# Kernel optimization log

Hardware: AMD Instinct MI355X
Metric: run time of the kernel (lower is better)

## Reference

```python
import jax, jax.numpy as jnp
import numpy as np
from jax import lax

_A = -0.75  # PyTorch bicubic coefficient


def _cubic_kernel(x):
    x = np.abs(x)
    return np.where(x <= 1.0, (_A + 2) * x**3 - (_A + 3) * x**2 + 1,
                    np.where(x < 2.0, _A * x**3 - 5 * _A * x**2 + 8 * _A * x - 4 * _A, 0.0))


def _cubic_mat(out_s, in_s):
    # align_corners=True bicubic interpolation matrix [out_s, in_s]
    i = np.arange(out_s)
    s = i * (in_s - 1) / (out_s - 1) if out_s > 1 else np.zeros(out_s)
    f = np.floor(s).astype(np.int64)
    t = s - f
    M = np.zeros((out_s, in_s), dtype=np.float32)
    for off in range(-1, 3):
        idx = np.clip(f + off, 0, in_s - 1)
        np.add.at(M, (i, idx), _cubic_kernel(t - off).astype(np.float32))
    return jnp.asarray(M)


def _bicubic_up(x, out_hw):
    Mh = _cubic_mat(out_hw[0], x.shape[-2])
    Mw = _cubic_mat(out_hw[1], x.shape[-1])
    y = jnp.einsum('Hh,bchw->bcHw', Mh, x)
    return jnp.einsum('Ww,bcHw->bcHW', Mw, y)


def _conv(x, w, b, pad=1):
    y = lax.conv_general_dilated(x, w, (1, 1), [(pad, pad), (pad, pad)],
                                 dimension_numbers=('NCHW', 'OIHW', 'NCHW'))
    return y + b[None, :, None, None]


def _pool(x):
    return lax.reduce_window(x, -jnp.inf, lax.max, (1, 1, 2, 2), (1, 1, 2, 2), 'VALID')


def _features(x, ws):
    # VGG19 feat1 = conv0+relu (64ch, full res); feat2 = conv2..conv14 (256ch, 1/4 res)
    x1 = jax.nn.relu(_conv(x, *ws[0]))
    h = jax.nn.relu(_conv(x1, *ws[1]))
    h = _pool(h)
    h = jax.nn.relu(_conv(h, *ws[2]))
    h = jax.nn.relu(_conv(h, *ws[3]))
    h = _pool(h)
    h = jax.nn.relu(_conv(h, *ws[4]))
    h = jax.nn.relu(_conv(h, *ws[5]))
    h = jax.nn.relu(_conv(h, *ws[6]))
    h = _bicubic_up(h, x1.shape[-2:])  # bicubic, align_corners=True
    return jnp.concatenate([x1, h], axis=1)  # 64 + 256 = 320 channels


def _forward(x_ref, x_template, w0, b0, w2, b2, w5, b5, w7, b7, w10, b10, w12, b12,
             w14, b14, coef_ref, coef_temp, fw1, fb1, fw2, fb2, fw3, fb3):
    ws = [(w0, b0), (w2, b2), (w5, b5), (w7, b7), (w10, b10), (w12, b12), (w14, b14)]
    fref = _features(x_ref, ws)
    ftem = _features(x_template, ws)
    # L2-normalize over channel dim
    fref = fref / (1e-8 + jnp.linalg.norm(fref, axis=1, keepdims=True))
    ftem = ftem / (1e-8 + jnp.linalg.norm(ftem, axis=1, keepdims=True))
    b, c, H, W = fref.shape
    fref = fref.reshape(b, c, H // 2, 2, W // 2, 2).mean(axis=(3, 5))
    # dense correlation volume
    dist = jnp.einsum('bcmn,bcpq->bmnpq', fref, ftem) / 320.0
    m, n, p, q = dist.shape[1:]
    dist = dist.reshape(b, m * n, p * q)
    # dual-axis softmax + sqrt combination (LoFTR-style)
    conf_ref = jax.nn.softmax(coef_ref * dist, axis=-2)
    conf_tmp = jax.nn.softmax(coef_temp * dist, axis=-1)
    confidence = jnp.sqrt(conf_ref * conf_tmp)
    conf_values, _ = lax.top_k(confidence, 5)  # [b, m*n, 5]
    conf = conf_values.reshape(b, m, n, 5).transpose(0, 3, 1, 2)
    # final head (dropout = identity in eval)
    h = jax.nn.relu(_conv(conf, fw1, fb1))
    h = jax.nn.relu(_conv(h, fw2, fb2))
    out = _conv(h, fw3, fb3, pad=0)
    out = _bicubic_up(out, x_ref.shape[-2:])
    return out


def setup_inputs() -> dict:
    key = jax.random.key(0)
    ks = jax.random.split(key, 16)
    B, H, W = 1, 128, 128

    def cw(k, o, i, s):
        return jax.random.normal(k, (o, i, s, s), jnp.float32) * (1.0 / np.sqrt(i * s * s))

    d = {
        'x_ref': jax.random.normal(ks[0], (B, 3, H, W), jnp.float32),
        'x_template': jax.random.normal(ks[1], (B, 3, H, W), jnp.float32),
        'w0': cw(ks[2], 64, 3, 3), 'b0': jnp.zeros((64,), jnp.float32),
        'w2': cw(ks[3], 64, 64, 3), 'b2': jnp.zeros((64,), jnp.float32),
        'w5': cw(ks[4], 128, 64, 3), 'b5': jnp.zeros((128,), jnp.float32),
        'w7': cw(ks[5], 128, 128, 3), 'b7': jnp.zeros((128,), jnp.float32),
        'w10': cw(ks[6], 256, 128, 3), 'b10': jnp.zeros((256,), jnp.float32),
        'w12': cw(ks[7], 256, 256, 3), 'b12': jnp.zeros((256,), jnp.float32),
        'w14': cw(ks[8], 256, 256, 3), 'b14': jnp.zeros((256,), jnp.float32),
        'coef_ref': jnp.float32(1.0), 'coef_temp': jnp.float32(1.0),
        # final head: weights_init_normal -> N(1/3, 0.02)
        'fw1': 1.0 / 3 + 0.02 * jax.random.normal(ks[9], (8, 5, 3, 3), jnp.float32),
        'fb1': 0.02 * jax.random.normal(ks[10], (8,), jnp.float32),
        'fw2': 1.0 / 3 + 0.02 * jax.random.normal(ks[11], (8, 8, 3, 3), jnp.float32),
        'fb2': 0.02 * jax.random.normal(ks[12], (8,), jnp.float32),
        'fw3': 1.0 / 3 + 0.02 * jax.random.normal(ks[13], (1, 8, 1, 1), jnp.float32),
        'fb3': 0.02 * jax.random.normal(ks[14], (1,), jnp.float32),
    }
    return d


def reference(x_ref, x_template, w0, b0, w2, b2, w5, b5, w7, b7, w10, b10, w12, b12,
              w14, b14, coef_ref, coef_temp, fw1, fb1, fw2, fb2, fw3, fb3):
    return _forward(x_ref, x_template, w0, b0, w2, b2, w5, b5, w7, b7, w10, b10,
                    w12, b12, w14, b14, coef_ref, coef_temp, fw1, fb1, fw2, fb2, fw3, fb3)
```

## Files before the change

kernel.cpp:

```cpp
#include <hip/hip_runtime.h>
#include <math.h>

typedef unsigned short ushort_t;
typedef unsigned int uint_t;
typedef __attribute__((ext_vector_type(8))) short bf16x8;
typedef __attribute__((ext_vector_type(4))) float f32x4;

#define FSTRIDE ((size_t)16384 * 320)
#define TSTRIDE ((size_t)16384 * 64)

__device__ inline ushort_t f2bf(float f) {
    union { float f; uint_t u; } x; x.f = f;
    uint_t r = x.u + 0x7fffu + ((x.u >> 16) & 1u);
    return (ushort_t)(r >> 16);
}
__device__ inline float bf2f(ushort_t h) {
    union { uint_t u; float f; } x; x.u = ((uint_t)h) << 16;
    return x.f;
}
__device__ inline float bflo(uint_t u) {
    union { uint_t u; float f; } x; x.u = u << 16; return x.f;
}
__device__ inline float bfhi(uint_t u) {
    union { uint_t u; float f; } x; x.u = u & 0xffff0000u; return x.f;
}

__global__ void wtrans_k(const float* __restrict__ w, ushort_t* __restrict__ wT, int CO, int CI)
{
    int idx = blockIdx.x * 256 + threadIdx.x;
    if (idx >= CO * CI * 9) return;
    int tap = idx % 9;
    int rem = idx / 9;
    int ci = rem % CI;
    int co = rem / CI;
    wT[((size_t)tap * CO + co) * CI + ci] = f2bf(w[idx]);
}

__global__ __launch_bounds__(256) void conv0_k(const float* __restrict__ x0, const float* __restrict__ x1,
                                               const float* __restrict__ w,
                                               const float* __restrict__ b, ushort_t* __restrict__ F)
{
    const float* x = blockIdx.y ? x1 : x0;
    F += (size_t)blockIdx.y * FSTRIDE;
    int co = threadIdx.x & 63;
    int p = blockIdx.x * 4 + (threadIdx.x >> 6);
    int y = p >> 7, xx = p & 127;
    float acc = b[co];
#pragma unroll
    for (int ci = 0; ci < 3; ++ci) {
#pragma unroll
        for (int t = 0; t < 9; ++t) {
            int dy = t / 3 - 1, dx = t % 3 - 1;
            int yy = y + dy, xc = xx + dx;
            if ((unsigned)yy < 128u && (unsigned)xc < 128u) {
                acc += x[ci * 16384 + yy * 128 + xc] * w[co * 27 + ci * 9 + t];
            }
        }
    }
    F[(size_t)p * 320 + co] = f2bf(fmaxf(acc, 0.f));
}

template<int CI>
__global__ __launch_bounds__(256) void conv_mfma_k(
    const ushort_t* __restrict__ in, int ldin, int inoff, size_t inImgStride,
    const ushort_t* __restrict__ wT, const float* __restrict__ bias,
    ushort_t* __restrict__ out, int ldout, int outoff, size_t outImgStride,
    int H, int W, int CO)
{
    in += (size_t)blockIdx.z * inImgStride;
    out += (size_t)blockIdx.z * outImgStride;
    const int tid = threadIdx.x;
    const int lane = tid & 63, wid = tid >> 6;
    const int wr = wid >> 1, wc = wid & 1;
    const int m0 = blockIdx.x * 64;
    const int n0 = blockIdx.y * 64;
    const int fr = lane & 15;
    const int fo = (lane >> 4) << 3;

    size_t abase[2];
    unsigned vmask[2];
#pragma unroll
    for (int mi = 0; mi < 2; ++mi) {
        int p = m0 + wr * 32 + mi * 16 + fr;
        int y = p / W, x = p % W;
        abase[mi] = (size_t)p * ldin + inoff + fo;
        unsigned vm = 0;
#pragma unroll
        for (int t = 0; t < 9; ++t) {
            int dy = t / 3 - 1, dx = t % 3 - 1;
            if ((unsigned)(y + dy) < (unsigned)H && (unsigned)(x + dx) < (unsigned)W) vm |= 1u << t;
        }
        vmask[mi] = vm;
    }

    f32x4 zero = {0.f, 0.f, 0.f, 0.f};
    f32x4 acc[2][2] = {{zero, zero}, {zero, zero}};
    const bf16x8 zz = {0, 0, 0, 0, 0, 0, 0, 0};

    for (int t = 0; t < 9; ++t) {
        int toff = ((t / 3 - 1) * W + (t % 3 - 1)) * ldin;
        bool v0 = (vmask[0] >> t) & 1u;
        bool v1 = (vmask[1] >> t) & 1u;
        const ushort_t* wp0 = wT + ((size_t)(t * CO + n0 + wc * 32 + fr)) * CI + fo;
        const ushort_t* wp1 = wp0 + (size_t)16 * CI;
#pragma unroll
        for (int kc = 0; kc < CI / 32; ++kc) {
            int k0 = kc * 32;
            bf16x8 a0 = v0 ? *(const bf16x8*)(in + abase[0] + toff + k0) : zz;
            bf16x8 a1 = v1 ? *(const bf16x8*)(in + abase[1] + toff + k0) : zz;
            bf16x8 b0 = *(const bf16x8*)(wp0 + k0);
            bf16x8 b1 = *(const bf16x8*)(wp1 + k0);
            acc[0][0] = __builtin_amdgcn_mfma_f32_16x16x32_bf16(a0, b0, acc[0][0], 0, 0, 0);
            acc[0][1] = __builtin_amdgcn_mfma_f32_16x16x32_bf16(a0, b1, acc[0][1], 0, 0, 0);
            acc[1][0] = __builtin_amdgcn_mfma_f32_16x16x32_bf16(a1, b0, acc[1][0], 0, 0, 0);
            acc[1][1] = __builtin_amdgcn_mfma_f32_16x16x32_bf16(a1, b1, acc[1][1], 0, 0, 0);
        }
    }

#pragma unroll
    for (int mi = 0; mi < 2; ++mi) {
#pragma unroll
        for (int ni = 0; ni < 2; ++ni) {
            int row0 = m0 + wr * 32 + mi * 16 + ((lane >> 4) << 2);
            int col = n0 + wc * 32 + ni * 16 + (lane & 15);
            float bv = bias[col];
#pragma unroll
            for (int r = 0; r < 4; ++r)
                out[(size_t)(row0 + r) * ldout + outoff + col] = f2bf(fmaxf(acc[mi][ni][r] + bv, 0.f));
        }
    }
}

__global__ void maxpool_nhwc_k(const ushort_t* __restrict__ in, ushort_t* __restrict__ out,
                               int C, int Hi, int Wi)
{
    in += (size_t)blockIdx.y * TSTRIDE;
    out += (size_t)blockIdx.y * TSTRIDE;
    int idx = blockIdx.x * 256 + threadIdx.x;
    int CG = C >> 3;
    int Wo = Wi >> 1, Ho = Hi >> 1;
    if (idx >= Ho * Wo * CG) return;
    int cg = idx % CG;
    int p = idx / CG;
    int y = p / Wo, x = p % Wo;
    const ushort_t* ip = in + ((size_t)(2 * y) * Wi + 2 * x) * C + cg * 8;
    bf16x8 v0 = *(const bf16x8*)(ip);
    bf16x8 v1 = *(const bf16x8*)(ip + C);
    bf16x8 v2 = *(const bf16x8*)(ip + (size_t)Wi * C);
    bf16x8 v3 = *(const bf16x8*)(ip + (size_t)Wi * C + C);
    bf16x8 r;
#pragma unroll
    for (int j = 0; j < 8; ++j) {
        float m = fmaxf(fmaxf(bf2f((ushort_t)v0[j]), bf2f((ushort_t)v1[j])),
                        fmaxf(bf2f((ushort_t)v2[j]), bf2f((ushort_t)v3[j])));
        r[j] = (short)f2bf(m);
    }
    *(bf16x8*)(out + (size_t)p * C + cg * 8) = r;
}

__device__ inline void cubw(float t, float* w) {
    float x0 = 1.f + t, x2 = 1.f - t, x3 = 2.f - t;
    w[0] = ((-0.75f*x0 + 3.75f)*x0 - 6.f)*x0 + 3.f;
    w[1] = (1.25f*t - 2.25f)*t*t + 1.f;
    w[2] = (1.25f*x2 - 2.25f)*x2*x2 + 1.f;
    w[3] = ((-0.75f*x3 + 3.75f)*x3 - 6.f)*x3 + 3.f;
}

__global__ __launch_bounds__(256) void bicubic_nhwc_k(const ushort_t* __restrict__ in, ushort_t* __restrict__ F)
{
    in += (size_t)blockIdx.y * TSTRIDE;
    F += (size_t)blockIdx.y * FSTRIDE;
    int idx = blockIdx.x * 256 + threadIdx.x;
    int cg = idx & 31;
    int p = idx >> 5;
    int Y = p >> 7, X = p & 127;
    float sy = (float)Y * (31.f / 127.f);
    float sx = (float)X * (31.f / 127.f);
    int fy = (int)floorf(sy), fx = (int)floorf(sx);
    float ty = sy - (float)fy, tx = sx - (float)fx;
    float wy[4], wx[4];
    cubw(ty, wy); cubw(tx, wx);
    float a[8] = {0.f, 0.f, 0.f, 0.f, 0.f, 0.f, 0.f, 0.f};
#pragma unroll
    for (int i = 0; i < 4; ++i) {
        int yy = min(max(fy - 1 + i, 0), 31);
#pragma unroll
        for (int j = 0; j < 4; ++j) {
            int xx = min(max(fx - 1 + j, 0), 31);
            float w = wy[i] * wx[j];
            bf16x8 v = *(const bf16x8*)(in + ((size_t)yy * 32 + xx) * 256 + cg * 8);
#pragma unroll
            for (int e = 0; e < 8; ++e) a[e] += w * bf2f((ushort_t)v[e]);
        }
    }
    bf16x8 r;
#pragma unroll
    for (int e = 0; e < 8; ++e) r[e] = (short)f2bf(a[e]);
    *(bf16x8*)(F + (size_t)p * 320 + 64 + cg * 8) = r;
}

__global__ __launch_bounds__(256) void norm_k(ushort_t* __restrict__ F)
{
    int lane = threadIdx.x & 63;
    int p = blockIdx.x * 4 + (threadIdx.x >> 6);
    ushort_t* rp = F + (size_t)p * 320;
    bool act = lane < 40;
    bf16x8 v = {0, 0, 0, 0, 0, 0, 0, 0};
    float ss = 0.f;
    if (act) {
        v = *(const bf16x8*)(rp + lane * 8);
#pragma unroll
        for (int e = 0; e < 8; ++e) { float f = bf2f((ushort_t)v[e]); ss += f * f; }
    }
#pragma unroll
    for (int off = 32; off > 0; off >>= 1) ss += __shfl_xor(ss, off);
    float inv = 1.f / (1e-8f + sqrtf(ss));
    if (act) {
#pragma unroll
        for (int e = 0; e < 8; ++e) v[e] = (short)f2bf(bf2f((ushort_t)v[e]) * inv);
        *(bf16x8*)(rp + lane * 8) = v;
    }
}

__global__ void pool_ref_nhwc_k(const ushort_t* __restrict__ F, ushort_t* __restrict__ A)
{
    int idx = blockIdx.x * 256 + threadIdx.x;
    if (idx >= 4096 * 40) return;
    int cg = idx % 40;
    int m = idx / 40;
    int y = m >> 6, x = m & 63;
    const ushort_t* ip = F + ((size_t)(2 * y) * 128 + 2 * x) * 320 + cg * 8;
    bf16x8 v0 = *(const bf16x8*)(ip);
    bf16x8 v1 = *(const bf16x8*)(ip + 320);
    bf16x8 v2 = *(const bf16x8*)(ip + 128 * 320);
    bf16x8 v3 = *(const bf16x8*)(ip + 128 * 320 + 320);
    bf16x8 r;
#pragma unroll
    for (int j = 0; j < 8; ++j) {
        float s = bf2f((ushort_t)v0[j]) + bf2f((ushort_t)v1[j]) + bf2f((ushort_t)v2[j]) + bf2f((ushort_t)v3[j]);
        r[j] = (short)f2bf(0.25f * s);
    }
    *(bf16x8*)(A + (size_t)m * 320 + cg * 8) = r;
}

__global__ __launch_bounds__(256) void gemm_corr_k(
    const ushort_t* __restrict__ A, const ushort_t* __restrict__ B, ushort_t* __restrict__ D,
    const float* __restrict__ coefr, const float* __restrict__ coeft,
    float* __restrict__ rpsum, float* __restrict__ cpsum)
{
    __shared__ ushort_t lA[128 * 32];
    __shared__ ushort_t lB[128 * 32];
    __shared__ float cl[2][128];
    __shared__ float rl[2][128];
    const int tid = threadIdx.x;
    const int lane = tid & 63;
    const int wid = tid >> 6;
    const int wr = wid >> 1, wc = wid & 1;
    const int m0 = blockIdx.y * 128, n0 = blockIdx.x * 128;
    const int rS = tid >> 2;
    const int cS = (tid & 3) << 3;
    const int fr = lane & 15;
    const int fo = (lane >> 4) << 3;

    f32x4 zero = {0.f, 0.f, 0.f, 0.f};
    f32x4 acc[4][4];
#pragma unroll
    for (int i = 0; i < 4; ++i)
#pragma unroll
        for (int j = 0; j < 4; ++j) acc[i][j] = zero;

    for (int k0 = 0; k0 < 320; k0 += 32) {
        uint4 a0 = *(const uint4*)(A + (size_t)(m0 + rS) * 320 + k0 + cS);
        uint4 a1 = *(const uint4*)(A + (size_t)(m0 + 64 + rS) * 320 + k0 + cS);
        uint4 b0 = *(const uint4*)(B + (size_t)(n0 + rS) * 320 + k0 + cS);
        uint4 b1 = *(const uint4*)(B + (size_t)(n0 + 64 + rS) * 320 + k0 + cS);
        __syncthreads();
        *(uint4*)&lA[rS * 32 + cS] = a0;
        *(uint4*)&lA[(64 + rS) * 32 + cS] = a1;
        *(uint4*)&lB[rS * 32 + cS] = b0;
        *(uint4*)&lB[(64 + rS) * 32 + cS] = b1;
        __syncthreads();
        bf16x8 af[4], bfr[4];
#pragma unroll
        for (int mi = 0; mi < 4; ++mi)
            af[mi] = *(const bf16x8*)&lA[(wr * 64 + mi * 16 + fr) * 32 + fo];
#pragma unroll
        for (int ni = 0; ni < 4; ++ni)
            bfr[ni] = *(const bf16x8*)&lB[(wc * 64 + ni * 16 + fr) * 32 + fo];
#pragma unroll
        for (int mi = 0; mi < 4; ++mi)
#pragma unroll
            for (int ni = 0; ni < 4; ++ni)
                acc[mi][ni] = __builtin_amdgcn_mfma_f32_16x16x32_bf16(af[mi], bfr[ni], acc[mi][ni], 0, 0, 0);
    }

    const float s = 1.0f / 320.0f;
    const float cr = coefr[0], ct = coeft[0];
    float cp[4] = {0.f, 0.f, 0.f, 0.f};
    float rp[4][4];
#pragma unroll
    for (int mi = 0; mi < 4; ++mi)
#pragma unroll
        for (int r = 0; r < 4; ++r) rp[mi][r] = 0.f;

#pragma unroll
    for (int mi = 0; mi < 4; ++mi) {
#pragma unroll
        for (int ni = 0; ni < 4; ++ni) {
            int grow0 = m0 + wr * 64 + mi * 16 + ((lane >> 4) << 2);
            int gcol = n0 + wc * 64 + ni * 16 + (lane & 15);
#pragma unroll
            for (int r = 0; r < 4; ++r) {
                float d = acc[mi][ni][r] * s;
                D[(size_t)(grow0 + r) * 16384 + gcol] = f2bf(d);
                cp[ni] += __expf(cr * d);
                rp[mi][r] += __expf(ct * d);
            }
        }
    }
#pragma unroll
    for (int ni = 0; ni < 4; ++ni) {
        cp[ni] += __shfl_xor(cp[ni], 16);
        cp[ni] += __shfl_xor(cp[ni], 32);
    }
    if (lane < 16) {
#pragma unroll
        for (int ni = 0; ni < 4; ++ni)
            cl[wr][wc * 64 + ni * 16 + lane] = cp[ni];
    }
#pragma unroll
    for (int mi = 0; mi < 4; ++mi)
#pragma unroll
        for (int r = 0; r < 4; ++r) {
            rp[mi][r] += __shfl_xor(rp[mi][r], 1);
            rp[mi][r] += __shfl_xor(rp[mi][r], 2);
            rp[mi][r] += __shfl_xor(rp[mi][r], 4);
            rp[mi][r] += __shfl_xor(rp[mi][r], 8);
        }
    if ((lane & 15) == 0) {
        int g = lane >> 4;
#pragma unroll
        for (int mi = 0; mi < 4; ++mi)
#pragma unroll
            for (int r = 0; r < 4; ++r)
                rl[wc][wr * 64 + mi * 16 + g * 4 + r] = rp[mi][r];
    }
    __syncthreads();
    if (tid < 128) {
        cpsum[(size_t)blockIdx.y * 16384 + n0 + tid] = cl[0][tid] + cl[1][tid];
        rpsum[(size_t)blockIdx.x * 4096 + m0 + tid] = rl[0][tid] + rl[1][tid];
    }
}

__global__ void colfin_k(const float* __restrict__ cpsum, float* __restrict__ lc)
{
    int j = blockIdx.x * 256 + threadIdx.x;
    float s = 0.f;
#pragma unroll
    for (int k = 0; k < 32; ++k) s += cpsum[(size_t)k * 16384 + j];
    lc[j] = -0.5f * __logf(s);
}
__global__ void rowfin_k(const float* __restrict__ rpsum, float* __restrict__ invr)
{
    int m = blockIdx.x * 256 + threadIdx.x;
    float s = 0.f;
#pragma unroll
    for (int k = 0; k < 128; ++k) s += rpsum[(size_t)k * 4096 + m];
    invr[m] = rsqrtf(s);
}

#define INS5(w_) { float w = (w_); float mx; \
    mx = fmaxf(w, t0); w = fminf(w, t0); t0 = mx; \
    mx = fmaxf(w, t1); w = fminf(w, t1); t1 = mx; \
    mx = fmaxf(w, t2); w = fminf(w, t2); t2 = mx; \
    mx = fmaxf(w, t3); w = fminf(w, t3); t3 = mx; \
    t4 = fmaxf(w, t4); }

__global__ __launch_bounds__(256) void row_topk_k(
    const ushort_t* __restrict__ Dist, const float* __restrict__ lc,
    const float* __restrict__ invr,
    const float* __restrict__ coefr, const float* __restrict__ coeft,
    float* __restrict__ conf5)
{
    int wid = threadIdx.x >> 6, lane = threadIdx.x & 63;
    int row = blockIdx.x * 4 + wid;
    float hc = 0.5f * (coefr[0] + coeft[0]);
    const ushort_t* rp = Dist + (size_t)row * 16384;

    float t0 = -1e30f, t1 = -1e30f, t2 = -1e30f, t3 = -1e30f, t4 = -1e30f;
    for (int i = 0; i < 32; ++i) {
        int col = (i * 64 + lane) * 8;
        uint4 u = *(const uint4*)(rp + col);
        float4 l0 = *(const float4*)(lc + col);
        float4 l1 = *(const float4*)(lc + col + 4);
        INS5(fmaf(hc, bflo(u.x), l0.x));
        INS5(fmaf(hc, bfhi(u.x), l0.y));
        INS5(fmaf(hc, bflo(u.y), l0.z));
        INS5(fmaf(hc, bfhi(u.y), l0.w));
        INS5(fmaf(hc, bflo(u.z), l1.x));
        INS5(fmaf(hc, bfhi(u.z), l1.y));
        INS5(fmaf(hc, bflo(u.w), l1.z));
        INS5(fmaf(hc, bfhi(u.w), l1.w));
    }
#pragma unroll
    for (int off = 1; off < 64; off <<= 1) {
        float o0 = __shfl_xor(t0, off), o1 = __shfl_xor(t1, off), o2 = __shfl_xor(t2, off);
        float o3 = __shfl_xor(t3, off), o4 = __shfl_xor(t4, off);
        INS5(o0); INS5(o1); INS5(o2); INS5(o3); INS5(o4);
    }
    if (lane == 0) {
        float iv = invr[row];
        conf5[0 * 4096 + row] = __expf(t0) * iv;
        conf5[1 * 4096 + row] = __expf(t1) * iv;
        conf5[2 * 4096 + row] = __expf(t2) * iv;
        conf5[3 * 4096 + row] = __expf(t3) * iv;
        conf5[4 * 4096 + row] = __expf(t4) * iv;
    }
}

__global__ void conv3x3_k(const float* __restrict__ in, const float* __restrict__ wgt,
                          const float* __restrict__ bias, float* __restrict__ out,
                          int Cin, int H, int W, int relu)
{
    int p = blockIdx.x * 256 + threadIdx.x;
    int HW = H * W;
    if (p >= HW) return;
    int co0 = blockIdx.y * 8;
    int y = p / W, x = p - y * W;
    float acc0 = bias[co0+0], acc1 = bias[co0+1], acc2 = bias[co0+2], acc3 = bias[co0+3];
    float acc4 = bias[co0+4], acc5 = bias[co0+5], acc6 = bias[co0+6], acc7 = bias[co0+7];
    bool ym = y > 0, yp = y < H-1, xm = x > 0, xp = x < W-1;
    for (int ci = 0; ci < Cin; ++ci) {
        const float* ip = in + (size_t)ci * HW + p;
        float v0 = (ym && xm) ? ip[-W-1] : 0.f;
        float v1 = (ym)       ? ip[-W]   : 0.f;
        float v2 = (ym && xp) ? ip[-W+1] : 0.f;
        float v3 = (xm)       ? ip[-1]   : 0.f;
        float v4 =              ip[0];
        float v5 = (xp)       ? ip[1]    : 0.f;
        float v6 = (yp && xm) ? ip[W-1]  : 0.f;
        float v7 = (yp)       ? ip[W]    : 0.f;
        float v8 = (yp && xp) ? ip[W+1]  : 0.f;
        const float* wp = wgt + ((size_t)co0 * Cin + ci) * 9;
        size_t ws = (size_t)Cin * 9;
#define CACC(q, a) { const float* wq = wp + q * ws; \
        a += wq[0]*v0 + wq[1]*v1 + wq[2]*v2 + wq[3]*v3 + wq[4]*v4 \
           + wq[5]*v5 + wq[6]*v6 + wq[7]*v7 + wq[8]*v8; }
        CACC(0, acc0) CACC(1, acc1) CACC(2, acc2) CACC(3, acc3)
        CACC(4, acc4) CACC(5, acc5) CACC(6, acc6) CACC(7, acc7)
#undef CACC
    }
#define CW(q, a) { float r = a; if (relu) r = fmaxf(r, 0.f); out[(size_t)(co0+q)*HW + p] = r; }
    CW(0, acc0) CW(1, acc1) CW(2, acc2) CW(3, acc3)
    CW(4, acc4) CW(5, acc5) CW(6, acc6) CW(7, acc7)
#undef CW
}

__global__ void bicubic_k(const float* __restrict__ in, float* __restrict__ out,
                          int C, int Hin, int Win, int Hout, int Wout)
{
    int idx = blockIdx.x * 256 + threadIdx.x;
    int total = C * Hout * Wout;
    if (idx >= total) return;
    int X = idx % Wout;
    int Y = (idx / Wout) % Hout;
    int c = idx / (Wout * Hout);
    float sy = (float)Y * (float)(Hin - 1) / (float)(Hout - 1);
    float sx = (float)X * (float)(Win - 1) / (float)(Wout - 1);
    int fy = (int)floorf(sy), fx = (int)floorf(sx);
    float ty = sy - (float)fy, tx = sx - (float)fx;
    float wy[4], wx[4];
    cubw(ty, wy); cubw(tx, wx);
    const float* ip = in + (size_t)c * Hin * Win;
    float acc = 0.f;
#pragma unroll
    for (int i = 0; i < 4; ++i) {
        int yy = min(max(fy - 1 + i, 0), Hin - 1);
        float ra = 0.f;
#pragma unroll
        for (int j = 0; j < 4; ++j) {
            int xx = min(max(fx - 1 + j, 0), Win - 1);
            ra += wx[j] * ip[yy * Win + xx];
        }
        acc += wy[i] * ra;
    }
    out[idx] = acc;
}

__global__ void conv1x1_k(const float* __restrict__ in, const float* __restrict__ w,
                          const float* __restrict__ b, float* __restrict__ out, int Cin, int HW)
{
    int p = blockIdx.x * 256 + threadIdx.x;
    if (p >= HW) return;
    float a = b[0];
    for (int c = 0; c < Cin; ++c) a += w[c] * in[(size_t)c * HW + p];
    out[p] = a;
}

extern "C" void kernel_launch(void* const* d_in, const int* in_sizes, int n_in,
                              void* d_out, int out_size, void* d_ws, size_t ws_size,
                              hipStream_t stream)
{
    const float* x_ref = (const float*)d_in[0];
    const float* x_tem = (const float*)d_in[1];
    const float* w0  = (const float*)d_in[2];   const float* b0  = (const float*)d_in[3];
    const float* w2  = (const float*)d_in[4];   const float* b2  = (const float*)d_in[5];
    const float* w5  = (const float*)d_in[6];   const float* b5  = (const float*)d_in[7];
    const float* w7  = (const float*)d_in[8];   const float* b7  = (const float*)d_in[9];
    const float* w10 = (const float*)d_in[10];  const float* b10 = (const float*)d_in[11];
    const float* w12 = (const float*)d_in[12];  const float* b12 = (const float*)d_in[13];
    const float* w14 = (const float*)d_in[14];  const float* b14 = (const float*)d_in[15];
    const float* coefr = (const float*)d_in[16];
    const float* coeft = (const float*)d_in[17];
    const float* fw1 = (const float*)d_in[18];  const float* fb1 = (const float*)d_in[19];
    const float* fw2 = (const float*)d_in[20];  const float* fb2 = (const float*)d_in[21];
    const float* fw3 = (const float*)d_in[22];  const float* fb3 = (const float*)d_in[23];
    float* out = (float*)d_out;

    char* wsp = (char*)d_ws;
    auto alloc = [&](size_t bytes) { char* p = wsp; wsp += (bytes + 255) & ~(size_t)255; return p; };
    ushort_t* F     = (ushort_t*)alloc(2 * FSTRIDE * 2);
    ushort_t* t1    = (ushort_t*)alloc(2 * TSTRIDE * 2);
    ushort_t* t2    = (ushort_t*)alloc(2 * TSTRIDE * 2);
    ushort_t* wT2   = (ushort_t*)alloc((size_t)64 * 64 * 9 * 2);
    ushort_t* wT5   = (ushort_t*)alloc((size_t)128 * 64 * 9 * 2);
    ushort_t* wT7   = (ushort_t*)alloc((size_t)128 * 128 * 9 * 2);
    ushort_t* wT10  = (ushort_t*)alloc((size_t)256 * 128 * 9 * 2);
    ushort_t* wT12  = (ushort_t*)alloc((size_t)256 * 256 * 9 * 2);
    ushort_t* wT14  = (ushort_t*)alloc((size_t)256 * 256 * 9 * 2);
    ushort_t* Abuf  = (ushort_t*)alloc((size_t)4096 * 320 * 2);
    ushort_t* dist  = (ushort_t*)alloc((size_t)4096 * 16384 * 2);
    float*    rpsum = (float*)alloc((size_t)128 * 4096 * 4);
    float*    cpsum = (float*)alloc((size_t)32 * 16384 * 4);
    float*    lc    = (float*)alloc(16384 * 4);
    float*    invr  = (float*)alloc(4096 * 4);
    float*    conf5 = (float*)alloc(5 * 4096 * 4);
    float*    h1    = (float*)alloc(8 * 4096 * 4);
    float*    h2    = (float*)alloc(8 * 4096 * 4);
    float*    out64 = (float*)alloc(4096 * 4);
    (void)ws_size; (void)n_in; (void)in_sizes; (void)out_size;

    wtrans_k<<<(64*64*9 + 255)/256, 256, 0, stream>>>(w2, wT2, 64, 64);
    wtrans_k<<<(128*64*9 + 255)/256, 256, 0, stream>>>(w5, wT5, 128, 64);
    wtrans_k<<<(128*128*9 + 255)/256, 256, 0, stream>>>(w7, wT7, 128, 128);
    wtrans_k<<<(256*128*9 + 255)/256, 256, 0, stream>>>(w10, wT10, 256, 128);
    wtrans_k<<<(256*256*9 + 255)/256, 256, 0, stream>>>(w12, wT12, 256, 256);
    wtrans_k<<<(256*256*9 + 255)/256, 256, 0, stream>>>(w14, wT14, 256, 256);

    conv0_k<<<dim3(4096, 2), 256, 0, stream>>>(x_ref, x_tem, w0, b0, F);
    conv_mfma_k<64><<<dim3(256, 1, 2), 256, 0, stream>>>(F, 320, 0, FSTRIDE, wT2, b2, t1, 64, 0, TSTRIDE, 128, 128, 64);
    maxpool_nhwc_k<<<dim3(128, 2), 256, 0, stream>>>(t1, t2, 64, 128, 128);
    conv_mfma_k<64><<<dim3(64, 2, 2), 256, 0, stream>>>(t2, 64, 0, TSTRIDE, wT5, b5, t1, 128, 0, TSTRIDE, 64, 64, 128);
    conv_mfma_k<128><<<dim3(64, 2, 2), 256, 0, stream>>>(t1, 128, 0, TSTRIDE, wT7, b7, t2, 128, 0, TSTRIDE, 64, 64, 128);
    maxpool_nhwc_k<<<dim3(64, 2), 256, 0, stream>>>(t2, t1, 128, 64, 64);
    conv_mfma_k<128><<<dim3(16, 4, 2), 256, 0, stream>>>(t1, 128, 0, TSTRIDE, wT10, b10, t2, 256, 0, TSTRIDE, 32, 32, 256);
    conv_mfma_k<256><<<dim3(16, 4, 2), 256, 0, stream>>>(t2, 256, 0, TSTRIDE, wT12, b12, t1, 256, 0, TSTRIDE, 32, 32, 256);
    conv_mfma_k<256><<<dim3(16, 4, 2), 256, 0, stream>>>(t1, 256, 0, TSTRIDE, wT14, b14, t2, 256, 0, TSTRIDE, 32, 32, 256);
    bicubic_nhwc_k<<<dim3(2048, 2), 256, 0, stream>>>(t2, F);
    norm_k<<<8192, 256, 0, stream>>>(F);

    pool_ref_nhwc_k<<<640, 256, 0, stream>>>(F, Abuf);

    gemm_corr_k<<<dim3(128, 32), 256, 0, stream>>>(Abuf, F + FSTRIDE, dist, coefr, coeft, rpsum, cpsum);

    colfin_k<<<64, 256, 0, stream>>>(cpsum, lc);
    rowfin_k<<<16, 256, 0, stream>>>(rpsum, invr);

    row_topk_k<<<1024, 256, 0, stream>>>(dist, lc, invr, coefr, coeft, conf5);

    conv3x3_k<<<dim3(16, 1), 256, 0, stream>>>(conf5, fw1, fb1, h1, 5, 64, 64, 1);
    conv3x3_k<<<dim3(16, 1), 256, 0, stream>>>(h1, fw2, fb2, h2, 8, 64, 64, 1);
    conv1x1_k<<<16, 256, 0, stream>>>(h2, fw3, fb3, out64, 8, 4096);
    bicubic_k<<<64, 256, 0, stream>>>(out64, out, 1, 64, 64, 128, 128);
}
```

Baseline: 417.1 us.

## Transpose MFMA operands for vectorized stores, use direct-to-LDS loads in correlation GEMM

Swaps the A/B operands of the MFMA calls so each lane holds four consecutive output channels, which allows packed 8-byte stores of the bf16 conv outputs and of the correlation matrix instead of scattered 2-byte stores. The correlation GEMM now stages tiles with global_load_lds, bypassing registers, and adds a trailing barrier per k-step. When both coefficients are equal it reuses one set of exponentials for the row and column sums. The 1/4-resolution convs move to a new single-wave-per-block kernel with many more, smaller blocks to raise parallelism on the small 32x32 layers.

```diff
diff --git a/kernel.cpp b/kernel.cpp
--- a/kernel.cpp
+++ b/kernel.cpp
@@ -23,6 +23,16 @@
 }
 __device__ inline float bfhi(uint_t u) {
     union { uint_t u; float f; } x; x.u = u & 0xffff0000u; return x.f;
+}
+__device__ inline uint_t cvtpk_bf16(float lo, float hi) {
+    uint_t r;
+    asm volatile("v_cvt_pk_bf16_f32 %0, %1, %2" : "=v"(r) : "v"(lo), "v"(hi));
+    return r;
+}
+__device__ inline void gload16(const void* g, void* l) {
+    __builtin_amdgcn_global_load_lds(
+        (const __attribute__((address_space(1))) void*)g,
+        (__attribute__((address_space(3))) void*)l, 16, 0, 0);
 }
 
 __global__ void wtrans_k(const float* __restrict__ w, ushort_t* __restrict__ wT, int CO, int CI)
@@ -110,10 +120,10 @@
             bf16x8 a1 = v1 ? *(const bf16x8*)(in + abase[1] + toff + k0) : zz;
             bf16x8 b0 = *(const bf16x8*)(wp0 + k0);
             bf16x8 b1 = *(const bf16x8*)(wp1 + k0);
-            acc[0][0] = __builtin_amdgcn_mfma_f32_16x16x32_bf16(a0, b0, acc[0][0], 0, 0, 0);
-            acc[0][1] = __builtin_amdgcn_mfma_f32_16x16x32_bf16(a0, b1, acc[0][1], 0, 0, 0);
-            acc[1][0] = __builtin_amdgcn_mfma_f32_16x16x32_bf16(a1, b0, acc[1][0], 0, 0, 0);
-            acc[1][1] = __builtin_amdgcn_mfma_f32_16x16x32_bf16(a1, b1, acc[1][1], 0, 0, 0);
+            acc[0][0] = __builtin_amdgcn_mfma_f32_16x16x32_bf16(b0, a0, acc[0][0], 0, 0, 0);
+            acc[0][1] = __builtin_amdgcn_mfma_f32_16x16x32_bf16(b1, a0, acc[0][1], 0, 0, 0);
+            acc[1][0] = __builtin_amdgcn_mfma_f32_16x16x32_bf16(b0, a1, acc[1][0], 0, 0, 0);
+            acc[1][1] = __builtin_amdgcn_mfma_f32_16x16x32_bf16(b1, a1, acc[1][1], 0, 0, 0);
         }
     }
 
@@ -121,12 +131,91 @@
     for (int mi = 0; mi < 2; ++mi) {
 #pragma unroll
         for (int ni = 0; ni < 2; ++ni) {
-            int row0 = m0 + wr * 32 + mi * 16 + ((lane >> 4) << 2);
-            int col = n0 + wc * 32 + ni * 16 + (lane & 15);
-            float bv = bias[col];
-#pragma unroll
-            for (int r = 0; r < 4; ++r)
-                out[(size_t)(row0 + r) * ldout + outoff + col] = f2bf(fmaxf(acc[mi][ni][r] + bv, 0.f));
+            int pix = m0 + wr * 32 + mi * 16 + (lane & 15);
+            int ch = n0 + wc * 32 + ni * 16 + ((lane >> 4) << 2);
+            float4 bv = *(const float4*)(bias + ch);
+            float r0 = fmaxf(acc[mi][ni][0] + bv.x, 0.f);
+            float r1 = fmaxf(acc[mi][ni][1] + bv.y, 0.f);
+            float r2 = fmaxf(acc[mi][ni][2] + bv.z, 0.f);
+            float r3 = fmaxf(acc[mi][ni][3] + bv.w, 0.f);
+            uint2 pk;
+            pk.x = (uint_t)f2bf(r0) | ((uint_t)f2bf(r1) << 16);
+            pk.y = (uint_t)f2bf(r2) | ((uint_t)f2bf(r3) << 16);
+            *(uint2*)(out + (size_t)pix * ldout + outoff + ch) = pk;
+        }
+    }
+}
+
+template<int CI>
+__global__ __launch_bounds__(64) void conv_mfma1w_k(
+    const ushort_t* __restrict__ in, int ldin, size_t inImgStride,
+    const ushort_t* __restrict__ wT, const float* __restrict__ bias,
+    ushort_t* __restrict__ out, int ldout, size_t outImgStride,
+    int H, int W, int CO)
+{
+    in += (size_t)blockIdx.z * inImgStride;
+    out += (size_t)blockIdx.z * outImgStride;
+    const int lane = threadIdx.x;
+    const int m0 = blockIdx.x * 32;
+    const int n0 = blockIdx.y * 32;
+    const int fr = lane & 15;
+    const int fo = (lane >> 4) << 3;
+
+    size_t abase[2];
+    unsigned vmask[2];
+#pragma unroll
+    for (int mi = 0; mi < 2; ++mi) {
+        int p = m0 + mi * 16 + fr;
+        int y = p / W, x = p % W;
+        abase[mi] = (size_t)p * ldin + fo;
+        unsigned vm = 0;
+#pragma unroll
+        for (int t = 0; t < 9; ++t) {
+            int dy = t / 3 - 1, dx = t % 3 - 1;
+            if ((unsigned)(y + dy) < (unsigned)H && (unsigned)(x + dx) < (unsigned)W) vm |= 1u << t;
+        }
+        vmask[mi] = vm;
+    }
+
+    f32x4 zero = {0.f, 0.f, 0.f, 0.f};
+    f32x4 acc[2][2] = {{zero, zero}, {zero, zero}};
+    const bf16x8 zz = {0, 0, 0, 0, 0, 0, 0, 0};
+
+    for (int t = 0; t < 9; ++t) {
+        int toff = ((t / 3 - 1) * W + (t % 3 - 1)) * ldin;
+        bool v0 = (vmask[0] >> t) & 1u;
+        bool v1 = (vmask[1] >> t) & 1u;
+        const ushort_t* wp0 = wT + ((size_t)(t * CO + n0 + fr)) * CI + fo;
+        const ushort_t* wp1 = wp0 + (size_t)16 * CI;
+#pragma unroll
+        for (int kc = 0; kc < CI / 32; ++kc) {
+            int k0 = kc * 32;
+            bf16x8 a0 = v0 ? *(const bf16x8*)(in + abase[0] + toff + k0) : zz;
+            bf16x8 a1 = v1 ? *(const bf16x8*)(in + abase[1] + toff + k0) : zz;
+            bf16x8 b0 = *(const bf16x8*)(wp0 + k0);
+            bf16x8 b1 = *(const bf16x8*)(wp1 + k0);
+            acc[0][0] = __builtin_amdgcn_mfma_f32_16x16x32_bf16(b0, a0, acc[0][0], 0, 0, 0);
+            acc[0][1] = __builtin_amdgcn_mfma_f32_16x16x32_bf16(b1, a0, acc[0][1], 0, 0, 0);
+            acc[1][0] = __builtin_amdgcn_mfma_f32_16x16x32_bf16(b0, a1, acc[1][0], 0, 0, 0);
+            acc[1][1] = __builtin_amdgcn_mfma_f32_16x16x32_bf16(b1, a1, acc[1][1], 0, 0, 0);
+        }
+    }
+
+#pragma unroll
+    for (int mi = 0; mi < 2; ++mi) {
+#pragma unroll
+        for (int ni = 0; ni < 2; ++ni) {
+            int pix = m0 + mi * 16 + (lane & 15);
+            int ch = n0 + ni * 16 + ((lane >> 4) << 2);
+            float4 bv = *(const float4*)(bias + ch);
+            float r0 = fmaxf(acc[mi][ni][0] + bv.x, 0.f);
+            float r1 = fmaxf(acc[mi][ni][1] + bv.y, 0.f);
+            float r2 = fmaxf(acc[mi][ni][2] + bv.z, 0.f);
+            float r3 = fmaxf(acc[mi][ni][3] + bv.w, 0.f);
+            uint2 pk;
+            pk.x = (uint_t)f2bf(r0) | ((uint_t)f2bf(r1) << 16);
+            pk.y = (uint_t)f2bf(r2) | ((uint_t)f2bf(r3) << 16);
+            *(uint2*)(out + (size_t)pix * ldout + ch) = pk;
         }
     }
 }
@@ -257,10 +346,19 @@
     const int wid = tid >> 6;
     const int wr = wid >> 1, wc = wid & 1;
     const int m0 = blockIdx.y * 128, n0 = blockIdx.x * 128;
-    const int rS = tid >> 2;
-    const int cS = (tid & 3) << 3;
     const int fr = lane & 15;
     const int fo = (lane >> 4) << 3;
+    const int srow = tid >> 2;
+    const int scol = (tid & 3) << 3;
+
+    const ushort_t* Ag0 = A + (size_t)(m0 + srow) * 320 + scol;
+    const ushort_t* Ag1 = Ag0 + (size_t)64 * 320;
+    const ushort_t* Bg0 = B + (size_t)(n0 + srow) * 320 + scol;
+    const ushort_t* Bg1 = Bg0 + (size_t)64 * 320;
+    ushort_t* lA0 = lA + wid * 512;
+    ushort_t* lA1 = lA + 2048 + wid * 512;
+    ushort_t* lB0 = lB + wid * 512;
+    ushort_t* lB1 = lB + 2048 + wid * 512;
 
     f32x4 zero = {0.f, 0.f, 0.f, 0.f};
     f32x4 acc[4][4];
@@ -270,15 +368,10 @@
         for (int j = 0; j < 4; ++j) acc[i][j] = zero;
 
     for (int k0 = 0; k0 < 320; k0 += 32) {
-        uint4 a0 = *(const uint4*)(A + (size_t)(m0 + rS) * 320 + k0 + cS);
-        uint4 a1 = *(const uint4*)(A + (size_t)(m0 + 64 + rS) * 320 + k0 + cS);
-        uint4 b0 = *(const uint4*)(B + (size_t)(n0 + rS) * 320 + k0 + cS);
-        uint4 b1 = *(const uint4*)(B + (size_t)(n0 + 64 + rS) * 320 + k0 + cS);
-        __syncthreads();
-        *(uint4*)&lA[rS * 32 + cS] = a0;
-        *(uint4*)&lA[(64 + rS) * 32 + cS] = a1;
-        *(uint4*)&lB[rS * 32 + cS] = b0;
-        *(uint4*)&lB[(64 + rS) * 32 + cS] = b1;
+        gload16(Ag0 + k0, lA0);
+        gload16(Ag1 + k0, lA1);
+        gload16(Bg0 + k0, lB0);
+        gload16(Bg1 + k0, lB1);
         __syncthreads();
         bf16x8 af[4], bfr[4];
 #pragma unroll
@@ -291,59 +384,73 @@
         for (int mi = 0; mi < 4; ++mi)
 #pragma unroll
             for (int ni = 0; ni < 4; ++ni)
-                acc[mi][ni] = __builtin_amdgcn_mfma_f32_16x16x32_bf16(af[mi], bfr[ni], acc[mi][ni], 0, 0, 0);
+                acc[mi][ni] = __builtin_amdgcn_mfma_f32_16x16x32_bf16(bfr[ni], af[mi], acc[mi][ni], 0, 0, 0);
+        __syncthreads();
     }
 
     const float s = 1.0f / 320.0f;
     const float cr = coefr[0], ct = coeft[0];
-    float cp[4] = {0.f, 0.f, 0.f, 0.f};
-    float rp[4][4];
-#pragma unroll
-    for (int mi = 0; mi < 4; ++mi)
-#pragma unroll
-        for (int r = 0; r < 4; ++r) rp[mi][r] = 0.f;
-
+    const bool sameCoef = (cr == ct);
+    float rpx[4] = {0.f, 0.f, 0.f, 0.f};
+    float cpx[4][4];
+#pragma unroll
+    for (int ni = 0; ni < 4; ++ni)
+#pragma unroll
+        for (int r = 0; r < 4; ++r) cpx[ni][r] = 0.f;
+
+    const int mrow = lane & 15;
+    const int ng = (lane >> 4) << 2;
 #pragma unroll
     for (int mi = 0; mi < 4; ++mi) {
+        int m = m0 + wr * 64 + mi * 16 + mrow;
+        ushort_t* drow = D + (size_t)m * 16384;
 #pragma unroll
         for (int ni = 0; ni < 4; ++ni) {
-            int grow0 = m0 + wr * 64 + mi * 16 + ((lane >> 4) << 2);
-            int gcol = n0 + wc * 64 + ni * 16 + (lane & 15);
-#pragma unroll
-            for (int r = 0; r < 4; ++r) {
-                float d = acc[mi][ni][r] * s;
-                D[(size_t)(grow0 + r) * 16384 + gcol] = f2bf(d);
-                cp[ni] += __expf(cr * d);
-                rp[mi][r] += __expf(ct * d);
+            int n = n0 + wc * 64 + ni * 16 + ng;
+            float d0 = acc[mi][ni][0] * s;
+            float d1 = acc[mi][ni][1] * s;
+            float d2 = acc[mi][ni][2] * s;
+            float d3 = acc[mi][ni][3] * s;
+            uint2 pk;
+            pk.x = cvtpk_bf16(d0, d1);
+            pk.y = cvtpk_bf16(d2, d3);
+            *(uint2*)(drow + n) = pk;
+            float e0 = __expf(cr * d0), e1 = __expf(cr * d1);
+            float e2 = __expf(cr * d2), e3 = __expf(cr * d3);
+            cpx[ni][0] += e0; cpx[ni][1] += e1; cpx[ni][2] += e2; cpx[ni][3] += e3;
+            if (sameCoef) {
+                rpx[mi] += e0 + e1 + e2 + e3;
+            } else {
+                rpx[mi] += __expf(ct * d0) + __expf(ct * d1) + __expf(ct * d2) + __expf(ct * d3);
             }
         }
     }
 #pragma unroll
-    for (int ni = 0; ni < 4; ++ni) {
-        cp[ni] += __shfl_xor(cp[ni], 16);
-        cp[ni] += __shfl_xor(cp[ni], 32);
+    for (int mi = 0; mi < 4; ++mi) {
+        rpx[mi] += __shfl_xor(rpx[mi], 16);
+        rpx[mi] += __shfl_xor(rpx[mi], 32);
     }
     if (lane < 16) {
 #pragma unroll
-        for (int ni = 0; ni < 4; ++ni)
-            cl[wr][wc * 64 + ni * 16 + lane] = cp[ni];
-    }
-#pragma unroll
-    for (int mi = 0; mi < 4; ++mi)
+        for (int mi = 0; mi < 4; ++mi)
+            rl[wc][wr * 64 + mi * 16 + lane] = rpx[mi];
+    }
+#pragma unroll
+    for (int ni = 0; ni < 4; ++ni)
 #pragma unroll
         for (int r = 0; r < 4; ++r) {
-            rp[mi][r] += __shfl_xor(rp[mi][r], 1);
-            rp[mi][r] += __shfl_xor(rp[mi][r], 2);
-            rp[mi][r] += __shfl_xor(rp[mi][r], 4);
-            rp[mi][r] += __shfl_xor(rp[mi][r], 8);
+            cpx[ni][r] += __shfl_xor(cpx[ni][r], 1);
+            cpx[ni][r] += __shfl_xor(cpx[ni][r], 2);
+            cpx[ni][r] += __shfl_xor(cpx[ni][r], 4);
+            cpx[ni][r] += __shfl_xor(cpx[ni][r], 8);
         }
     if ((lane & 15) == 0) {
         int g = lane >> 4;
 #pragma unroll
-        for (int mi = 0; mi < 4; ++mi)
+        for (int ni = 0; ni < 4; ++ni)
 #pragma unroll
             for (int r = 0; r < 4; ++r)
-                rl[wc][wr * 64 + mi * 16 + g * 4 + r] = rp[mi][r];
+                cl[wr][wc * 64 + ni * 16 + g * 4 + r] = cpx[ni][r];
     }
     __syncthreads();
     if (tid < 128) {
@@ -553,9 +660,9 @@
     conv_mfma_k<64><<<dim3(64, 2, 2), 256, 0, stream>>>(t2, 64, 0, TSTRIDE, wT5, b5, t1, 128, 0, TSTRIDE, 64, 64, 128);
     conv_mfma_k<128><<<dim3(64, 2, 2), 256, 0, stream>>>(t1, 128, 0, TSTRIDE, wT7, b7, t2, 128, 0, TSTRIDE, 64, 64, 128);
     maxpool_nhwc_k<<<dim3(64, 2), 256, 0, stream>>>(t2, t1, 128, 64, 64);
-    conv_mfma_k<128><<<dim3(16, 4, 2), 256, 0, stream>>>(t1, 128, 0, TSTRIDE, wT10, b10, t2, 256, 0, TSTRIDE, 32, 32, 256);
-    conv_mfma_k<256><<<dim3(16, 4, 2), 256, 0, stream>>>(t2, 256, 0, TSTRIDE, wT12, b12, t1, 256, 0, TSTRIDE, 32, 32, 256);
-    conv_mfma_k<256><<<dim3(16, 4, 2), 256, 0, stream>>>(t1, 256, 0, TSTRIDE, wT14, b14, t2, 256, 0, TSTRIDE, 32, 32, 256);
+    conv_mfma1w_k<128><<<dim3(32, 8, 2), 64, 0, stream>>>(t1, 128, TSTRIDE, wT10, b10, t2, 256, TSTRIDE, 32, 32, 256);
+    conv_mfma1w_k<256><<<dim3(32, 8, 2), 64, 0, stream>>>(t2, 256, TSTRIDE, wT12, b12, t1, 256, TSTRIDE, 32, 32, 256);
+    conv_mfma1w_k<256><<<dim3(32, 8, 2), 64, 0, stream>>>(t1, 256, TSTRIDE, wT14, b14, t2, 256, TSTRIDE, 32, 32, 256);
     bicubic_nhwc_k<<<dim3(2048, 2), 256, 0, stream>>>(t2, F);
     norm_k<<<8192, 256, 0, stream>>>(F);
 
```

Result: no change. 409.7 us (-1.8%).
